# Kernel tuning notes

Measured on AMD Instinct MI355X. Metric: run time of the kernel, lower is better.

Reference implementation:

```python
import jax, jax.numpy as jnp
import numpy as np

N, H, W, C = 4, 128, 128, 128
G = 8
GC = C // G
K = 9  # 3x3 deformable kernel
PAD = 1
HIN, WIN = H + 2 * PAD, W + 2 * PAD
EPS = 1e-5
OFFSET_SCALE = 1.0


def ln(x, g, b):
    m = jnp.mean(x, -1, keepdims=True)
    v = jnp.mean((x - m) ** 2, -1, keepdims=True)
    return (x - m) * jax.lax.rsqrt(v + EPS) * g + b


def gelu(x):
    return jax.nn.gelu(x, approximate=False)


def dcn_core(xp, offset, mask):
    # xp: (N,H,W,C) value features; offset: (N,H,W,G*K*2); mask: (N,H,W,G,K)
    xpad = jnp.pad(xp, ((0, 0), (PAD, PAD), (PAD, PAD), (0, 0)))
    img = xpad.reshape(N, HIN * WIN, G, GC)
    # reference points normalized by padded size (matches dcnv3_core_pytorch)
    ref_x = (jnp.arange(W, dtype=jnp.float32) + 1.5) / WIN  # (dil*(k-1))//2 + 0.5
    ref_y = (jnp.arange(H, dtype=jnp.float32) + 1.5) / HIN
    RX, RY = jnp.meshgrid(ref_x, ref_y)  # (H,W), xy indexing
    ref = jnp.stack([RX, RY], -1)  # (H,W,2) as (x,y)
    gx, gy = jnp.meshgrid(jnp.linspace(-1.0, 1.0, 3), jnp.linspace(-1.0, 1.0, 3), indexing='ij')
    grid = jnp.stack([gx / WIN, gy / HIN], -1).reshape(K, 2)  # dilation grid, x-major
    off = offset.reshape(N, H, W, G, K, 2)
    loc = (ref[None, :, :, None, None, :] + grid * OFFSET_SCALE
           + off * OFFSET_SCALE / jnp.array([WIN, HIN], jnp.float32))  # (N,H,W,G,K,2)
    # grid_sample align_corners=False pixel coords
    px = loc[..., 0] * WIN - 0.5
    py = loc[..., 1] * HIN - 0.5
    x0 = jnp.floor(px); y0 = jnp.floor(py)
    tx = px - x0; ty = py - y0
    x0i = x0.astype(jnp.int32); y0i = y0.astype(jnp.int32)
    x1i = x0i + 1; y1i = y0i + 1

    def gather(iy, ix):
        valid = ((iy >= 0) & (iy < HIN) & (ix >= 0) & (ix < WIN)).astype(xp.dtype)
        idx = jnp.clip(iy, 0, HIN - 1) * WIN + jnp.clip(ix, 0, WIN - 1)  # (N,H,W,G,K)
        idxf = idx.transpose(0, 1, 2, 4, 3).reshape(N, H * W * K, G, 1)
        v = jnp.take_along_axis(img, idxf, axis=1).reshape(N, H, W, K, G, GC)
        return v * valid.transpose(0, 1, 2, 4, 3)[..., None]

    acc = jnp.zeros((N, H, W, G, GC), xp.dtype)
    for iy, ix, wgt in ((y0i, x0i, (1 - ty) * (1 - tx)),
                        (y0i, x1i, (1 - ty) * tx),
                        (y1i, x0i, ty * (1 - tx)),
                        (y1i, x1i, ty * tx)):
        wm = (wgt * mask).transpose(0, 1, 2, 4, 3)[..., None]  # (N,H,W,K,G,1)
        acc = acc + jnp.sum(gather(iy, ix) * wm, axis=3)  # (N,H,W,G,GC)
    return acc.reshape(N, H, W, C)


def dcn(x, in_w, in_b, dw_k, dw_b, dwln_g, dwln_b, off_w, off_b, mask_w, mask_b, out_w, out_b):
    xp = x @ in_w + in_b  # input_proj
    # offset/mask branch: depthwise 3x3 conv on raw input, LN, GELU
    xc = jax.lax.conv_general_dilated(
        x, dw_k.reshape(3, 3, 1, C), (1, 1), 'SAME',
        dimension_numbers=('NHWC', 'HWIO', 'NHWC'), feature_group_count=C) + dw_b
    x1 = gelu(ln(xc, dwln_g, dwln_b))
    offset = x1 @ off_w + off_b  # (N,H,W,G*K*2)
    mask = jax.nn.softmax((x1 @ mask_w + mask_b).reshape(N, H, W, G, K), axis=-1)
    y = dcn_core(xp, offset, mask)
    return y @ out_w + out_b


def _forward(x, ln1_g, ln1_b, in_w, in_b, dw_k, dw_b, dwln_g, dwln_b, off_w, off_b,
             mask_w, mask_b, out_w, out_b, ln2_g, ln2_b, fc1_w, fc1_b, fc2_w, fc2_b):
    # pre-norm, no layer_scale, no drop_path (rate 0)
    x = x + dcn(ln(x, ln1_g, ln1_b), in_w, in_b, dw_k, dw_b, dwln_g, dwln_b,
                off_w, off_b, mask_w, mask_b, out_w, out_b)
    h = ln(x, ln2_g, ln2_b)
    h = gelu(h @ fc1_w + fc1_b) @ fc2_w + fc2_b
    return x + h


def setup_inputs() -> dict:
    key = jax.random.key(0)
    ks = jax.random.split(key, 10)

    def lin(k, fin, fout, scale=1.0):
        s = scale / np.sqrt(fin)
        return jax.random.uniform(k, (fin, fout), minval=-s, maxval=s, dtype=jnp.float32)

    d = {}
    d['x'] = jax.random.normal(ks[0], (N, H, W, C), dtype=jnp.float32)
    d['ln1_g'] = jnp.ones((C,), jnp.float32); d['ln1_b'] = jnp.zeros((C,), jnp.float32)
    d['in_w'] = lin(ks[1], C, C); d['in_b'] = jnp.zeros((C,), jnp.float32)
    d['dw_k'] = jax.random.normal(ks[2], (3, 3, C), dtype=jnp.float32) * 0.05
    d['dw_b'] = jnp.zeros((C,), jnp.float32)
    d['dwln_g'] = jnp.ones((C,), jnp.float32); d['dwln_b'] = jnp.zeros((C,), jnp.float32)
    d['off_w'] = lin(ks[3], C, G * K * 2, 0.1); d['off_b'] = jnp.zeros((G * K * 2,), jnp.float32)
    d['mask_w'] = lin(ks[4], C, G * K, 0.1); d['mask_b'] = jnp.zeros((G * K,), jnp.float32)
    d['out_w'] = lin(ks[5], C, C); d['out_b'] = jnp.zeros((C,), jnp.float32)
    d['ln2_g'] = jnp.ones((C,), jnp.float32); d['ln2_b'] = jnp.zeros((C,), jnp.float32)
    d['fc1_w'] = lin(ks[6], C, 4 * C); d['fc1_b'] = jnp.zeros((4 * C,), jnp.float32)
    d['fc2_w'] = lin(ks[7], 4 * C, C); d['fc2_b'] = jnp.zeros((C,), jnp.float32)
    return d


def reference(x, ln1_g, ln1_b, in_w, in_b, dw_k, dw_b, dwln_g, dwln_b, off_w, off_b,
              mask_w, mask_b, out_w, out_b, ln2_g, ln2_b, fc1_w, fc1_b, fc2_w, fc2_b):
    return _forward(x, ln1_g, ln1_b, in_w, in_b, dw_k, dw_b, dwln_g, dwln_b, off_w, off_b,
                    mask_w, mask_b, out_w, out_b, ln2_g, ln2_b, fc1_w, fc1_b, fc2_w, fc2_b)
```

## Files before the change

kernel.cpp:

```cpp
#include <hip/hip_runtime.h>
#include <hip/hip_bf16.h>
#include <math.h>

#define NB 4
#define HH 128
#define WW 128
#define CC 128
#define GG 8
#define GCC 16
#define KK 9
#define NHW (NB*HH*WW)

typedef __hip_bfloat16 bf16;
typedef __attribute__((ext_vector_type(8))) short short8;
typedef __attribute__((ext_vector_type(4))) float f32x4;

__device__ __forceinline__ float b2f(bf16 v){ return __bfloat162float(v); }
__device__ __forceinline__ bf16 f2b(float v){ return __float2bfloat16(v); }
__device__ __forceinline__ float gelu_f(float v){
  float x = fabsf(v) * 0.70710678118654752f;
  float t = __builtin_amdgcn_rcpf(fmaf(0.3275911f, x, 1.0f));
  float p = t*fmaf(t, fmaf(t, fmaf(t, fmaf(t, 1.061405429f, -1.453152027f),
                         1.421413741f), -0.284496736f), 0.254829592f);
  float e = __expf(-x*x);
  float er = copysignf(fmaf(-p, e, 1.0f), v);
  return 0.5f*v*(1.0f+er);
}
__device__ __forceinline__ float lo_bf(unsigned u){ union{unsigned i; float f;} c; c.i = u<<16; return c.f; }
__device__ __forceinline__ float hi_bf(unsigned u){ union{unsigned i; float f;} c; c.i = u&0xffff0000u; return c.f; }
__device__ __forceinline__ unsigned pk(float a, float b){
  return ((unsigned)__bfloat16_as_ushort(f2b(b))<<16) | (unsigned)__bfloat16_as_ushort(f2b(a));
}
__device__ __forceinline__ void st_out(bf16* p, float v){ *p = f2b(v); }
__device__ __forceinline__ void st_out(float* p, float v){ *p = v; }
__device__ __forceinline__ void acc8(float* a, uint4 u, float w){
  a[0]+=w*lo_bf(u.x); a[1]+=w*hi_bf(u.x); a[2]+=w*lo_bf(u.y); a[3]+=w*hi_bf(u.y);
  a[4]+=w*lo_bf(u.z); a[5]+=w*hi_bf(u.z); a[6]+=w*lo_bf(u.w); a[7]+=w*hi_bf(u.w);
}

__global__ __launch_bounds__(256) void prep_k(
    const float* __restrict__ inw,  const float* __restrict__ outw,
    const float* __restrict__ fc1w, const float* __restrict__ fc2w,
    const float* __restrict__ offw, const float* __restrict__ offb,
    const float* __restrict__ maskw,const float* __restrict__ maskb,
    bf16* __restrict__ inwt, bf16* __restrict__ outwt,
    bf16* __restrict__ w1t,  bf16* __restrict__ w2t,
    bf16* __restrict__ wsw,  float* __restrict__ cw)
{
  int idx = blockIdx.x*256 + threadIdx.x;
  if (idx < 16384){
    int n = idx>>7, k = idx&127;
    inwt[idx] = f2b(inw[(size_t)k*128 + n]);
  } else if (idx < 32768){
    int i = idx-16384; int n = i>>7, k = i&127;
    outwt[i] = f2b(outw[(size_t)k*128 + n]);
  } else if (idx < 98304){
    int i = idx-32768; int n = i>>7, k = i&127;
    w1t[i] = f2b(fc1w[(size_t)k*512 + n]);
  } else if (idx < 163840){
    int i = idx-98304; int n = i>>9, k = i&511;
    w2t[i] = f2b(fc2w[(size_t)k*128 + n]);
  } else if (idx < 192512){
    int i = idx-163840; int nn = i>>7, k = i&127;
    float v = (nn<144) ? offw[(size_t)k*144+nn] : (nn<216 ? maskw[(size_t)k*72+(nn-144)] : 0.f);
    wsw[i] = f2b(v);
  } else if (idx < 192736){
    int i = idx-192512;
    cw[i] = (i<144) ? offb[i] : (i<216 ? maskb[i-144] : 0.f);
  }
}

__global__ __launch_bounds__(256) void ln_k(const float* __restrict__ X,
    const float* __restrict__ gam, const float* __restrict__ bet, bf16* __restrict__ Y)
{
  int lane = threadIdx.x & 63;
  int wid  = threadIdx.x >> 6;
  size_t pix = (size_t)blockIdx.x*4 + wid;
  const float* xp = X + pix*CC;
  int c0 = lane*2;
  float v0 = xp[c0], v1 = xp[c0+1];
  float s = v0+v1, ss = v0*v0+v1*v1;
  #pragma unroll
  for (int off=32; off>0; off>>=1){ s += __shfl_xor(s,off,64); ss += __shfl_xor(ss,off,64); }
  float mean = s*(1.f/CC);
  float var  = ss*(1.f/CC) - mean*mean;
  float rstd = rsqrtf(var + 1e-5f);
  float y0 = (v0-mean)*rstd*gam[c0]   + bet[c0];
  float y1 = (v1-mean)*rstd*gam[c0+1] + bet[c0+1];
  Y[pix*CC + c0]   = f2b(y0);
  Y[pix*CC + c0+1] = f2b(y1);
}

__global__ __launch_bounds__(256) void convln_k(const bf16* __restrict__ XN,
    const float* __restrict__ dwk, const float* __restrict__ dwb,
    const float* __restrict__ gam, const float* __restrict__ bet, bf16* __restrict__ X1)
{
  int tid = threadIdx.x;
  int px = tid>>4, cg = tid&15;
  int ch0 = cg*8;
  int pix = blockIdx.x*16 + px;
  int w = pix & (WW-1), h = (pix>>7)&(HH-1), n = pix>>14;
  float acc[8];
  {
    float4 b0 = *(const float4*)(dwb + ch0), b1 = *(const float4*)(dwb + ch0 + 4);
    acc[0]=b0.x; acc[1]=b0.y; acc[2]=b0.z; acc[3]=b0.w;
    acc[4]=b1.x; acc[5]=b1.y; acc[6]=b1.z; acc[7]=b1.w;
  }
  #pragma unroll
  for (int ky=0;ky<3;ky++){
    int yy = h+ky-1; if ((unsigned)yy>=(unsigned)HH) continue;
    #pragma unroll
    for (int kx=0;kx<3;kx++){
      int xx = w+kx-1; if ((unsigned)xx>=(unsigned)WW) continue;
      uint4 u = *(const uint4*)(XN + ((size_t)((n*HH+yy)*WW+xx))*CC + ch0);
      const float* wp = dwk + (ky*3+kx)*CC + ch0;
      float4 w0 = *(const float4*)wp; float4 w1 = *(const float4*)(wp+4);
      acc[0] += lo_bf(u.x)*w0.x; acc[1] += hi_bf(u.x)*w0.y;
      acc[2] += lo_bf(u.y)*w0.z; acc[3] += hi_bf(u.y)*w0.w;
      acc[4] += lo_bf(u.z)*w1.x; acc[5] += hi_bf(u.z)*w1.y;
      acc[6] += lo_bf(u.w)*w1.z; acc[7] += hi_bf(u.w)*w1.w;
    }
  }
  float s=0.f, ss=0.f;
  #pragma unroll
  for (int i=0;i<8;i++){ s += acc[i]; ss += acc[i]*acc[i]; }
  #pragma unroll
  for (int off=1; off<16; off<<=1){ s += __shfl_xor(s,off,64); ss += __shfl_xor(ss,off,64); }
  float mean=s*(1.f/CC), var=ss*(1.f/CC)-mean*mean, rstd=rsqrtf(var+1e-5f);
  float4 g0 = *(const float4*)(gam + ch0), g1 = *(const float4*)(gam + ch0 + 4);
  float4 be0 = *(const float4*)(bet + ch0), be1 = *(const float4*)(bet + ch0 + 4);
  float gv[8] = {g0.x,g0.y,g0.z,g0.w,g1.x,g1.y,g1.z,g1.w};
  float bv[8] = {be0.x,be0.y,be0.z,be0.w,be1.x,be1.y,be1.z,be1.w};
  float o[8];
  #pragma unroll
  for (int i=0;i<8;i++) o[i] = gelu_f((acc[i]-mean)*rstd*gv[i] + bv[i]);
  uint4 up; up.x = pk(o[0],o[1]); up.y = pk(o[2],o[3]); up.z = pk(o[4],o[5]); up.w = pk(o[6],o[7]);
  *(uint4*)(X1 + (size_t)pix*CC + ch0) = up;
}

#define OMS 226
__global__ __launch_bounds__(256) void samp_k(const bf16* __restrict__ X1,
    const bf16* __restrict__ XP,
    const bf16* __restrict__ wsw, const float* __restrict__ cw,
    bf16* __restrict__ Y)
{
  __shared__ bf16 oms[32*OMS];
  int tid = threadIdx.x;
  int pix0 = blockIdx.x*32;
  int wave = tid>>6, l = tid&63, lo16 = l&15, quad = l>>4;
  int nt0 = wave*4;
  int ntn = (wave==3) ? 2 : 4;
  short8 af[2][4];
  #pragma unroll
  for (int mt=0;mt<2;mt++)
    #pragma unroll
    for (int ks=0;ks<4;ks++)
      af[mt][ks] = *(const short8*)(X1 + (size_t)(pix0+mt*16+lo16)*128 + ks*32 + quad*8);
  f32x4 z = {0.f,0.f,0.f,0.f};
  f32x4 acc[2][4];
  #pragma unroll
  for (int mt=0;mt<2;mt++)
    #pragma unroll
    for (int t=0;t<4;t++) acc[mt][t]=z;
  for (int t=0;t<ntn;t++){
    int nt = nt0+t;
    #pragma unroll
    for (int ks=0;ks<4;ks++){
      short8 bfr = *(const short8*)(wsw + (size_t)(nt*16+lo16)*128 + ks*32 + quad*8);
      acc[0][t] = __builtin_amdgcn_mfma_f32_16x16x32_bf16(af[0][ks], bfr, acc[0][t], 0,0,0);
      acc[1][t] = __builtin_amdgcn_mfma_f32_16x16x32_bf16(af[1][ks], bfr, acc[1][t], 0,0,0);
    }
  }
  for (int t=0;t<ntn;t++){
    int col = (nt0+t)*16 + lo16;
    float bb = cw[col];
    #pragma unroll
    for (int mt=0;mt<2;mt++)
      #pragma unroll
      for (int r=0;r<4;r++)
        oms[(mt*16 + quad*4 + r)*OMS + col] = f2b(acc[mt][t][r] + bb);
  }
  __syncthreads();
  {
    int m = tid>>3, g = tid&7;
    int base = m*OMS + 144 + g*9;
    float sc[9]; float mx = -1e30f;
    #pragma unroll
    for (int k=0;k<9;k++){ sc[k] = b2f(oms[base+k]); mx = fmaxf(mx, sc[k]); }
    float sum = 0.f;
    #pragma unroll
    for (int k=0;k<9;k++){ sc[k] = expf(sc[k]-mx); sum += sc[k]; }
    float inv = 1.f/sum;
    #pragma unroll
    for (int k=0;k<9;k++) oms[base+k] = f2b(sc[k]*inv);
  }
  __syncthreads();
  int oct = tid&15, sl = tid>>4;
  int g = oct>>1;
  int ch = g*GCC + (oct&1)*8;
  int w0 = pix0 & (WW-1);
  int h  = (pix0>>7) & (HH-1);
  int n  = pix0>>14;
  const bf16* base = XP + (size_t)n*HH*WW*CC + ch;
  for (int it=0; it<2; it++){
    int m = it*16 + sl;
    int wc = w0 + m;
    const bf16* omrow = &oms[m*OMS];
    float a[8] = {0.f,0.f,0.f,0.f,0.f,0.f,0.f,0.f};
    #pragma unroll
    for (int k=0;k<9;k++){
      float offx = b2f(omrow[g*18 + 2*k]);
      float offy = b2f(omrow[g*18 + 2*k + 1]);
      float mk   = b2f(omrow[144 + g*9 + k]);
      float pxf = (float)(wc + (k/3) - 1) + offx;
      float pyf = (float)(h  + (k%3) - 1) + offy;
      float x0f = floorf(pxf), y0f = floorf(pyf);
      float txf = pxf-x0f,     tyf = pyf-y0f;
      int x0 = (int)x0f, y0 = (int)y0f;
      int x1i = x0+1,    y1i = y0+1;
      float vx0 = ((unsigned)x0 <(unsigned)WW)?1.f:0.f;
      float vx1 = ((unsigned)x1i<(unsigned)WW)?1.f:0.f;
      float vy0 = ((unsigned)y0 <(unsigned)HH)?1.f:0.f;
      float vy1 = ((unsigned)y1i<(unsigned)HH)?1.f:0.f;
      int cx0 = min(max(x0,0),WW-1),  cx1 = min(max(x1i,0),WW-1);
      int cy0 = min(max(y0,0),HH-1),  cy1 = min(max(y1i,0),HH-1);
      float w00=(1.f-tyf)*(1.f-txf)*mk*vy0*vx0, w01=(1.f-tyf)*txf*mk*vy0*vx1;
      float w10=tyf*(1.f-txf)*mk*vy1*vx0,       w11=tyf*txf*mk*vy1*vx1;
      uint4 u00 = *(const uint4*)(base + ((size_t)(cy0*WW+cx0))*CC);
      uint4 u01 = *(const uint4*)(base + ((size_t)(cy0*WW+cx1))*CC);
      uint4 u10 = *(const uint4*)(base + ((size_t)(cy1*WW+cx0))*CC);
      uint4 u11 = *(const uint4*)(base + ((size_t)(cy1*WW+cx1))*CC);
      acc8(a,u00,w00); acc8(a,u01,w01); acc8(a,u10,w10); acc8(a,u11,w11);
    }
    uint4 outp;
    outp.x = pk(a[0],a[1]); outp.y = pk(a[2],a[3]);
    outp.z = pk(a[4],a[5]); outp.w = pk(a[6],a[7]);
    *(uint4*)(Y + (size_t)(pix0+m)*CC + ch) = outp;
  }
}

template<typename OutT, bool RES>
__global__ __launch_bounds__(256) void gemm_mfma(const bf16* __restrict__ A,
    const bf16* __restrict__ Bt, const float* __restrict__ bias,
    const float* __restrict__ res, OutT* __restrict__ C)
{
  int tid = threadIdx.x;
  int wave = tid>>6, l = tid&63, lo16 = l&15, quad = l>>4;
  int m0 = blockIdx.y*256 + wave*64;
  int n0 = blockIdx.x*64;
  short8 bfr[4][4];
  #pragma unroll
  for (int ks=0;ks<4;ks++)
    #pragma unroll
    for (int nt=0;nt<4;nt++)
      bfr[ks][nt] = *(const short8*)(Bt + (size_t)(n0+nt*16+lo16)*128 + ks*32 + quad*8);
  f32x4 z = {0.f,0.f,0.f,0.f};
  f32x4 acc[4][4];
  #pragma unroll
  for (int mt=0;mt<4;mt++)
    #pragma unroll
    for (int nt=0;nt<4;nt++) acc[mt][nt]=z;
  #pragma unroll
  for (int ks=0;ks<4;ks++){
    short8 af[4];
    #pragma unroll
    for (int mt=0;mt<4;mt++)
      af[mt] = *(const short8*)(A + (size_t)(m0+mt*16+lo16)*128 + ks*32 + quad*8);
    #pragma unroll
    for (int nt=0;nt<4;nt++)
      #pragma unroll
      for (int mt=0;mt<4;mt++)
        acc[mt][nt] = __builtin_amdgcn_mfma_f32_16x16x32_bf16(af[mt], bfr[ks][nt], acc[mt][nt], 0,0,0);
  }
  #pragma unroll
  for (int mt=0;mt<4;mt++)
    #pragma unroll
    for (int nt=0;nt<4;nt++){
      int col = n0 + nt*16 + lo16;
      float bb = bias[col];
      #pragma unroll
      for (int r=0;r<4;r++){
        int row = m0 + mt*16 + quad*4 + r;
        float v = acc[mt][nt][r] + bb;
        if (RES) v += res[(size_t)row*128 + col];
        st_out(&C[(size_t)row*128 + col], v);
      }
    }
}

__global__ __launch_bounds__(256) void mlp_mfma(const float* __restrict__ X2,
    const float* __restrict__ lng, const float* __restrict__ lnb,
    const bf16* __restrict__ w1t, const float* __restrict__ b1,
    const bf16* __restrict__ w2t, const float* __restrict__ b2,
    float* __restrict__ OUT)
{
  __shared__ __align__(16) char smem[18432 + 17408];
  bf16* wsm = (bf16*)smem;
  bf16* ts  = (bf16*)(smem + 18432);
  int tid = threadIdx.x;
  int wave = tid>>6, l = tid&63, lo16 = l&15, quad = l>>4;
  int m0 = blockIdx.x*128;
  int t8 = tid*8;
  short8 a1[2][4];
  {
    float gv[32], bv[32];
    #pragma unroll
    for (int ks=0;ks<4;ks++){
      *(float4*)(gv+ks*8)   = *(const float4*)(lng + ks*32 + quad*8);
      *(float4*)(gv+ks*8+4) = *(const float4*)(lng + ks*32 + quad*8 + 4);
      *(float4*)(bv+ks*8)   = *(const float4*)(lnb + ks*32 + quad*8);
      *(float4*)(bv+ks*8+4) = *(const float4*)(lnb + ks*32 + quad*8 + 4);
    }
    #pragma unroll
    for (int mt=0;mt<2;mt++){
      int row = m0 + wave*32 + mt*16 + lo16;
      const float* xr = X2 + (size_t)row*128;
      float v[32];
      #pragma unroll
      for (int ks=0;ks<4;ks++){
        *(float4*)(v+ks*8)   = *(const float4*)(xr + ks*32 + quad*8);
        *(float4*)(v+ks*8+4) = *(const float4*)(xr + ks*32 + quad*8 + 4);
      }
      float s=0.f, ss=0.f;
      #pragma unroll
      for (int i=0;i<32;i++){ s += v[i]; ss += v[i]*v[i]; }
      s += __shfl_xor(s,16,64); ss += __shfl_xor(ss,16,64);
      s += __shfl_xor(s,32,64); ss += __shfl_xor(ss,32,64);
      float mean = s*(1.f/CC), var = ss*(1.f/CC)-mean*mean, rstd = rsqrtf(var+1e-5f);
      #pragma unroll
      for (int ks=0;ks<4;ks++){
        short8 t;
        #pragma unroll
        for (int j=0;j<8;j++)
          t[j] = (short)__bfloat16_as_ushort(f2b((v[ks*8+j]-mean)*rstd*gv[ks*8+j] + bv[ks*8+j]));
        a1[mt][ks] = t;
      }
    }
  }
  f32x4 z = {0.f,0.f,0.f,0.f};
  f32x4 acc2[2][8];
  #pragma unroll
  for (int mt=0;mt<2;mt++)
    #pragma unroll
    for (int nt=0;nt<8;nt++) acc2[mt][nt]=z;

  for (int c0=0;c0<512;c0+=64){
    __syncthreads();
    #pragma unroll
    for (int it=0;it<4;it++){
      int e = it*2048 + t8;
      *(uint4*)(&wsm[(e>>7)*136 + (e&127)]) =
          *(const uint4*)(w1t + (size_t)(c0 + (e>>7))*128 + (e&127));
    }
    __syncthreads();
    f32x4 acc1[2][4];
    #pragma unroll
    for (int mt=0;mt<2;mt++)
      #pragma unroll
      for (int nt=0;nt<4;nt++) acc1[mt][nt]=z;
    #pragma unroll
    for (int ks=0;ks<4;ks++)
      #pragma unroll
      for (int nt=0;nt<4;nt++){
        short8 bfr = *(const short8*)(&wsm[(nt*16+lo16)*136 + ks*32 + quad*8]);
        acc1[0][nt] = __builtin_amdgcn_mfma_f32_16x16x32_bf16(a1[0][ks], bfr, acc1[0][nt], 0,0,0);
        acc1[1][nt] = __builtin_amdgcn_mfma_f32_16x16x32_bf16(a1[1][ks], bfr, acc1[1][nt], 0,0,0);
      }
    #pragma unroll
    for (int mt=0;mt<2;mt++)
      #pragma unroll
      for (int nt=0;nt<4;nt++){
        float bb = b1[c0 + nt*16 + lo16];
        #pragma unroll
        for (int r=0;r<4;r++)
          ts[(wave*32 + mt*16 + quad*4 + r)*68 + nt*16 + lo16] = f2b(gelu_f(acc1[mt][nt][r] + bb));
      }
    __syncthreads();
    #pragma unroll
    for (int it=0;it<4;it++){
      int e = it*2048 + t8;
      *(uint4*)(&wsm[(e>>6)*72 + (e&63)]) =
          *(const uint4*)(w2t + (size_t)(e>>6)*512 + c0 + (e&63));
    }
    __syncthreads();
    #pragma unroll
    for (int ks2=0;ks2<2;ks2++){
      short8 a2[2];
      #pragma unroll
      for (int mt=0;mt<2;mt++)
        a2[mt] = *(const short8*)(&ts[(wave*32 + mt*16 + lo16)*68 + ks2*32 + quad*8]);
      #pragma unroll
      for (int nt2=0;nt2<8;nt2++){
        short8 bfr2 = *(const short8*)(&wsm[(nt2*16+lo16)*72 + ks2*32 + quad*8]);
        acc2[0][nt2] = __builtin_amdgcn_mfma_f32_16x16x32_bf16(a2[0], bfr2, acc2[0][nt2], 0,0,0);
        acc2[1][nt2] = __builtin_amdgcn_mfma_f32_16x16x32_bf16(a2[1], bfr2, acc2[1][nt2], 0,0,0);
      }
    }
  }
  #pragma unroll
  for (int mt=0;mt<2;mt++)
    #pragma unroll
    for (int nt=0;nt<8;nt++){
      int col = nt*16 + lo16;
      float bb = b2[col];
      #pragma unroll
      for (int r=0;r<4;r++){
        int row = m0 + wave*32 + mt*16 + quad*4 + r;
        float v = acc2[mt][nt][r] + bb + X2[(size_t)row*128 + col];
        OUT[(size_t)row*128 + col] = v;
      }
    }
}

extern "C" void kernel_launch(void* const* d_in, const int* in_sizes, int n_in,
                              void* d_out, int out_size, void* d_ws, size_t ws_size,
                              hipStream_t stream)
{
  const float* x    = (const float*)d_in[0];
  const float* ln1g = (const float*)d_in[1];
  const float* ln1b = (const float*)d_in[2];
  const float* inw  = (const float*)d_in[3];
  const float* inb  = (const float*)d_in[4];
  const float* dwk  = (const float*)d_in[5];
  const float* dwb  = (const float*)d_in[6];
  const float* dwlng= (const float*)d_in[7];
  const float* dwlnb= (const float*)d_in[8];
  const float* offw = (const float*)d_in[9];
  const float* offb = (const float*)d_in[10];
  const float* maskw= (const float*)d_in[11];
  const float* maskb= (const float*)d_in[12];
  const float* outw = (const float*)d_in[13];
  const float* outb = (const float*)d_in[14];
  const float* ln2g = (const float*)d_in[15];
  const float* ln2b = (const float*)d_in[16];
  const float* fc1w = (const float*)d_in[17];
  const float* fc1b = (const float*)d_in[18];
  const float* fc2w = (const float*)d_in[19];
  const float* fc2b = (const float*)d_in[20];
  float* out = (float*)d_out;

  bf16* ws = (bf16*)d_ws;
  const size_t S = (size_t)NHW*CC;
  bf16* xn = ws;
  bf16* xp = ws + S;
  bf16* x1 = ws + 2*S;
  bf16* y  = xn;
  float* x2 = out;
  bf16* inwt  = ws + 3*S;
  bf16* outwt = inwt + 128*128;
  bf16* w1t   = outwt + 128*128;
  bf16* w2t   = w1t + 512*128;
  bf16* wsw   = w2t + 128*512;
  float* cw   = (float*)(wsw + 224*128);

  prep_k<<<753, 256, 0, stream>>>(inw, outw, fc1w, fc2w, offw, offb, maskw, maskb,
                                  inwt, outwt, w1t, w2t, wsw, cw);
  ln_k<<<NHW/4, 256, 0, stream>>>(x, ln1g, ln1b, xn);
  gemm_mfma<bf16,false><<<dim3(2,256), 256, 0, stream>>>(xn, inwt, inb, nullptr, xp);
  convln_k<<<NHW/16, 256, 0, stream>>>(xn, dwk, dwb, dwlng, dwlnb, x1);
  samp_k<<<NHW/32, 256, 0, stream>>>(x1, xp, wsw, cw, y);
  gemm_mfma<float,true><<<dim3(2,256), 256, 0, stream>>>(y, outwt, outb, x, x2);
  mlp_mfma<<<NHW/128, 256, 0, stream>>>(x2, ln2g, ln2b, w1t, fc1b, w2t, fc2b, out);
}
```

Baseline: 290.3 us.

## Pre-pack MLP weights in MFMA fragment order and load directly from global

The prep kernel now writes fc1/fc2 weights already arranged in the per-lane MFMA B-fragment layout. The MLP kernel then reads each fragment with one 16-byte global load per lane instead of staging weight tiles through LDS. This removes four block-wide barriers and the LDS copy per hidden chunk, leaving only the GELU tile in shared memory, which may improve occupancy. In exchange every wave re-reads the weights from L2/L1 with no LDS reuse, and there is no explicit barrier between the ts writes and reads. Each wave only touches its own rows of ts, so the missing barrier is likely safe.

```diff
diff --git a/kernel.cpp b/kernel.cpp
--- a/kernel.cpp
+++ b/kernel.cpp
@@ -44,7 +44,7 @@
     const float* __restrict__ offw, const float* __restrict__ offb,
     const float* __restrict__ maskw,const float* __restrict__ maskb,
     bf16* __restrict__ inwt, bf16* __restrict__ outwt,
-    bf16* __restrict__ w1t,  bf16* __restrict__ w2t,
+    bf16* __restrict__ w1p,  bf16* __restrict__ w2p,
     bf16* __restrict__ wsw,  float* __restrict__ cw)
 {
   int idx = blockIdx.x*256 + threadIdx.x;
@@ -55,11 +55,17 @@
     int i = idx-16384; int n = i>>7, k = i&127;
     outwt[i] = f2b(outw[(size_t)k*128 + n]);
   } else if (idx < 98304){
-    int i = idx-32768; int n = i>>7, k = i&127;
-    w1t[i] = f2b(fc1w[(size_t)k*512 + n]);
+    int i = idx-32768;
+    int j = i&7, l = (i>>3)&63, nt = (i>>9)&3, ks = (i>>11)&3, c = i>>13;
+    int row = c*64 + nt*16 + (l&15);
+    int col = ks*32 + (l>>4)*8 + j;
+    w1p[i] = f2b(fc1w[(size_t)col*512 + row]);
   } else if (idx < 163840){
-    int i = idx-98304; int n = i>>9, k = i&511;
-    w2t[i] = f2b(fc2w[(size_t)k*128 + n]);
+    int i = idx-98304;
+    int j = i&7, l = (i>>3)&63, nt2 = (i>>9)&7, ks2 = (i>>12)&1, c = i>>13;
+    int hid = c*64 + ks2*32 + (l>>4)*8 + j;
+    int col = nt2*16 + (l&15);
+    w2p[i] = f2b(fc2w[(size_t)hid*128 + col]);
   } else if (idx < 192512){
     int i = idx-163840; int nn = i>>7, k = i&127;
     float v = (nn<144) ? offw[(size_t)k*144+nn] : (nn<216 ? maskw[(size_t)k*72+(nn-144)] : 0.f);
@@ -290,17 +296,15 @@
 
 __global__ __launch_bounds__(256) void mlp_mfma(const float* __restrict__ X2,
     const float* __restrict__ lng, const float* __restrict__ lnb,
-    const bf16* __restrict__ w1t, const float* __restrict__ b1,
-    const bf16* __restrict__ w2t, const float* __restrict__ b2,
+    const bf16* __restrict__ w1p, const float* __restrict__ b1,
+    const bf16* __restrict__ w2p, const float* __restrict__ b2,
     float* __restrict__ OUT)
 {
-  __shared__ __align__(16) char smem[18432 + 17408];
-  bf16* wsm = (bf16*)smem;
-  bf16* ts  = (bf16*)(smem + 18432);
+  __shared__ __align__(16) bf16 ts[128*68];
   int tid = threadIdx.x;
   int wave = tid>>6, l = tid&63, lo16 = l&15, quad = l>>4;
   int m0 = blockIdx.x*128;
-  int t8 = tid*8;
+  int l8 = l*8;
   short8 a1[2][4];
   {
     float gv[32], bv[32];
@@ -344,15 +348,10 @@
     #pragma unroll
     for (int nt=0;nt<8;nt++) acc2[mt][nt]=z;
 
-  for (int c0=0;c0<512;c0+=64){
-    __syncthreads();
-    #pragma unroll
-    for (int it=0;it<4;it++){
-      int e = it*2048 + t8;
-      *(uint4*)(&wsm[(e>>7)*136 + (e&127)]) =
-          *(const uint4*)(w1t + (size_t)(c0 + (e>>7))*128 + (e&127));
-    }
-    __syncthreads();
+  for (int c=0;c<8;c++){
+    const bf16* w1c = w1p + (size_t)c*8192;
+    const bf16* w2c = w2p + (size_t)c*8192;
+    int c0 = c*64;
     f32x4 acc1[2][4];
     #pragma unroll
     for (int mt=0;mt<2;mt++)
@@ -362,7 +361,7 @@
     for (int ks=0;ks<4;ks++)
       #pragma unroll
       for (int nt=0;nt<4;nt++){
-        short8 bfr = *(const short8*)(&wsm[(nt*16+lo16)*136 + ks*32 + quad*8]);
+        short8 bfr = *(const short8*)(w1c + (ks*4+nt)*512 + l8);
         acc1[0][nt] = __builtin_amdgcn_mfma_f32_16x16x32_bf16(a1[0][ks], bfr, acc1[0][nt], 0,0,0);
         acc1[1][nt] = __builtin_amdgcn_mfma_f32_16x16x32_bf16(a1[1][ks], bfr, acc1[1][nt], 0,0,0);
       }
@@ -375,14 +374,6 @@
         for (int r=0;r<4;r++)
           ts[(wave*32 + mt*16 + quad*4 + r)*68 + nt*16 + lo16] = f2b(gelu_f(acc1[mt][nt][r] + bb));
       }
-    __syncthreads();
-    #pragma unroll
-    for (int it=0;it<4;it++){
-      int e = it*2048 + t8;
-      *(uint4*)(&wsm[(e>>6)*72 + (e&63)]) =
-          *(const uint4*)(w2t + (size_t)(e>>6)*512 + c0 + (e&63));
-    }
-    __syncthreads();
     #pragma unroll
     for (int ks2=0;ks2<2;ks2++){
       short8 a2[2];
@@ -391,7 +382,7 @@
         a2[mt] = *(const short8*)(&ts[(wave*32 + mt*16 + lo16)*68 + ks2*32 + quad*8]);
       #pragma unroll
       for (int nt2=0;nt2<8;nt2++){
-        short8 bfr2 = *(const short8*)(&wsm[(nt2*16+lo16)*72 + ks2*32 + quad*8]);
+        short8 bfr2 = *(const short8*)(w2c + (ks2*8+nt2)*512 + l8);
         acc2[0][nt2] = __builtin_amdgcn_mfma_f32_16x16x32_bf16(a2[0], bfr2, acc2[0][nt2], 0,0,0);
         acc2[1][nt2] = __builtin_amdgcn_mfma_f32_16x16x32_bf16(a2[1], bfr2, acc2[1][nt2], 0,0,0);
       }
@@ -448,17 +439,17 @@
   float* x2 = out;
   bf16* inwt  = ws + 3*S;
   bf16* outwt = inwt + 128*128;
-  bf16* w1t   = outwt + 128*128;
-  bf16* w2t   = w1t + 512*128;
-  bf16* wsw   = w2t + 128*512;
+  bf16* w1p   = outwt + 128*128;
+  bf16* w2p   = w1p + 512*128;
+  bf16* wsw   = w2p + 128*512;
   float* cw   = (float*)(wsw + 224*128);
 
   prep_k<<<753, 256, 0, stream>>>(inw, outw, fc1w, fc2w, offw, offb, maskw, maskb,
-                                  inwt, outwt, w1t, w2t, wsw, cw);
+                                  inwt, outwt, w1p, w2p, wsw, cw);
   ln_k<<<NHW/4, 256, 0, stream>>>(x, ln1g, ln1b, xn);
   gemm_mfma<bf16,false><<<dim3(2,256), 256, 0, stream>>>(xn, inwt, inb, nullptr, xp);
   convln_k<<<NHW/16, 256, 0, stream>>>(xn, dwk, dwb, dwlng, dwlnb, x1);
   samp_k<<<NHW/32, 256, 0, stream>>>(x1, xp, wsw, cw, y);
   gemm_mfma<float,true><<<dim3(2,256), 256, 0, stream>>>(y, outwt, outb, x, x2);
-  mlp_mfma<<<NHW/128, 256, 0, stream>>>(x2, ln2g, ln2b, w1t, fc1b, w2t, fc2b, out);
-}
+  mlp_mfma<<<NHW/128, 256, 0, stream>>>(x2, ln2g, ln2b, w1p, fc1b, w2p, fc2b, out);
+}
```

After: 317.8 us. 1.09x slower.
